# Kernel tuning notes

Measured on AMD Instinct MI355X. Metric: run time of the kernel, lower is better.

The kernel has to match this reference:

```python
import jax, jax.numpy as jnp
import numpy as np

LOCAL_EMB = 16  # local_emb_size: neighbors gathered per point


def _linear_params(key, fan_in, fan_out):
    kw, kb = jax.random.split(key)
    lim = 1.0 / np.sqrt(fan_in)
    W = jax.random.uniform(kw, (fan_in, fan_out), minval=-lim, maxval=lim, dtype=jnp.float32)
    b = jax.random.uniform(kb, (fan_out,), minval=-lim, maxval=lim, dtype=jnp.float32)
    return W, b


def setup_inputs() -> dict:
    key = jax.random.key(0)
    ks = jax.random.split(key, 4)
    M, K = 1024, 128
    windows = jax.random.normal(ks[0], (M, K, 3), dtype=jnp.float32)
    W1, b1 = _linear_params(ks[1], 3, 32)
    W2, b2 = _linear_params(ks[2], 32, 64)
    W3, b3 = _linear_params(ks[3], 64, 128)
    return {"windows": windows, "W1": W1, "b1": b1, "W2": W2, "b2": b2, "W3": W3, "b3": b3}


def reference(windows, W1, b1, W2, b2, W3, b3):
    # windows: (M, K, 3)
    M, K, _ = windows.shape
    # --- knn_points(windows, windows, K=LOCAL_EMB): per-window pairwise sq dists ---
    sq = jnp.sum(windows * windows, axis=-1)                      # (M, K)
    d2 = sq[:, :, None] + sq[:, None, :] - 2.0 * jnp.einsum('mkc,mjc->mkj', windows, windows)  # (M,K,K)
    _, idx = jax.lax.top_k(-d2, LOCAL_EMB)                        # (M, K, LOCAL_EMB) nearest (incl. self)
    grouped = jax.vmap(lambda pts, i: pts[i])(windows, idx)       # (M, K, LOCAL_EMB, 3)
    # --- center on query point ---
    rel = grouped - windows[:, :, None, :]                        # (M, K, LOCAL_EMB, 3)
    # --- n_scale_batch: normalize each neighborhood by its max radius ---
    scale = jnp.max(jnp.linalg.norm(rel, axis=-1), axis=-1, keepdims=True)  # (M, K, 1)
    rel = rel / jnp.maximum(scale, 1e-8)[..., None]
    # --- GraphConv: per-neighbor MLP stack then max over neighbors ---
    h = jax.nn.relu(rel @ W1 + b1)                                # (M, K, LOCAL_EMB, 32)
    h = jax.nn.relu(h @ W2 + b2)                                  # (M, K, LOCAL_EMB, 64)
    h = h @ W3 + b3                                               # (M, K, LOCAL_EMB, 128)
    return jnp.max(h, axis=-2)                                    # (M, K, 128)
```

## Files before the change

kernel.cpp:

```cpp
#include <hip/hip_runtime.h>

typedef __bf16 bf16x8 __attribute__((ext_vector_type(8)));
typedef __bf16 bf16x2 __attribute__((ext_vector_type(2)));
typedef float  f32x4  __attribute__((ext_vector_type(4)));
typedef float  f32x2  __attribute__((ext_vector_type(2)));
typedef unsigned long long u64;

#define MFMA(a, b, c) __builtin_amdgcn_mfma_f32_16x16x32_bf16((a), (b), (c), 0, 0, 0)

__device__ __forceinline__ f32x2 fma2(f32x2 a, f32x2 b, f32x2 c) {
    return __builtin_elementwise_fma(a, b, c);
}
__device__ __forceinline__ f32x2 relu2(f32x2 a) {
    f32x2 z = {0.0f, 0.0f};
    return __builtin_elementwise_max(a, z);
}
__device__ __forceinline__ void hilo2(f32x2 h, unsigned& hiw, unsigned& low) {
    bf16x2 hb = __builtin_convertvector(h, bf16x2);
    unsigned hw = __builtin_bit_cast(unsigned, hb);
    f32x2 hf;
    hf[0] = __builtin_bit_cast(float, hw << 16);
    hf[1] = __builtin_bit_cast(float, hw & 0xFFFF0000u);
    f32x2 lo = h - hf;
    bf16x2 lb = __builtin_convertvector(lo, bf16x2);
    hiw = hw;
    low = __builtin_bit_cast(unsigned, lb);
}
__device__ __forceinline__ bf16x8 frag4(unsigned w0, unsigned w1, unsigned w2, unsigned w3) {
    uint4 u; u.x = w0; u.y = w1; u.z = w2; u.w = w3;
    return __builtin_bit_cast(bf16x8, u);
}

__global__ __launch_bounds__(256) void miniemb_kernel(
    const float* __restrict__ windows,
    const float* __restrict__ W1, const float* __restrict__ b1,
    const float* __restrict__ W2, const float* __restrict__ b2,
    const float* __restrict__ W3, const float* __restrict__ b3,
    float* __restrict__ out)
{
    __shared__ float relbuf[48 * 128];
    __shared__ uint4 w3lds[16][64];

    float (*pts4)[4] = reinterpret_cast<float(*)[4]>(&w3lds[0][0]);

    const int m    = blockIdx.x;
    const int tid  = threadIdx.x;
    const int w    = tid >> 6;
    const int lane = tid & 63;
    const int g    = lane >> 4;
    const int ln   = lane & 15;

    const float* wm = windows + (size_t)m * 128 * 3;
    if (tid < 128) {
        float x = wm[tid * 3], y = wm[tid * 3 + 1], z = wm[tid * 3 + 2];
        float s = __fadd_rn(__fadd_rn(__fmul_rn(x, x), __fmul_rn(y, y)),
                            __fmul_rn(z, z));
        f32x4 P = {x, y, z, s};
        *(f32x4*)&pts4[tid][0] = P;
    }
    __syncthreads();

    const int k = tid >> 1;
    const int h = tid & 1;
    f32x4 Q = *(const f32x4*)&pts4[k][0];
    u64 bd[16];
    #pragma unroll
    for (int t = 0; t < 16; ++t) bd[t] = ~0ull;
    #pragma unroll 1
    for (int jj = 0; jj < 64; ++jj) {
        const int j = (h << 6) + jj;
        f32x4 P = *(const f32x4*)&pts4[j][0];
        float dot = __fadd_rn(__fadd_rn(__fmul_rn(Q.x, P.x),
                                        __fmul_rn(Q.y, P.y)),
                              __fmul_rn(Q.z, P.z));
        float dd = __fsub_rn(__fadd_rn(Q.w, P.w), __fmul_rn(2.0f, dot));
        unsigned u = __float_as_uint(dd);
        unsigned key32 = u ^ (((unsigned)(((int)u) >> 31)) | 0x80000000u);
        u64 kk = ((u64)key32 << 32) | (unsigned)j;
        bool ct[16];
        #pragma unroll
        for (int t = 0; t < 16; ++t) ct[t] = bd[t] < kk;
        #pragma unroll
        for (int t = 15; t >= 1; --t)
            bd[t] = ct[t] ? bd[t] : (ct[t - 1] ? kk : bd[t - 1]);
        bd[0] = ct[0] ? bd[0] : kk;
    }

    unsigned msk = 0;
    #pragma unroll
    for (int i = 0; i < 16; ++i) {
        u64 o = __shfl_xor(bd[15 - i], 1);
        msk |= (bd[i] < o) ? (1u << i) : 0u;
    }
    const int cnt   = __popc(msk);
    const int rbase = h ? (16 - cnt) : 0;

    float m2 = 0.0f;
    #pragma unroll
    for (int i = 0; i < 16; ++i) {
        if (i < cnt) {
            f32x4 P = *(const f32x4*)&pts4[(unsigned)bd[i] & 127u][0];
            float dx = P.x - Q.x, dy = P.y - Q.y, dz = P.z - Q.z;
            m2 = fmaxf(m2, dx * dx + dy * dy + dz * dz);
        }
    }
    m2 = fmaxf(m2, __shfl_xor(m2, 1));
    const float inv = 1.0f / fmaxf(sqrtf(m2), 1e-8f);

    #pragma unroll
    for (int i = 0; i < 16; ++i) {
        if (i < cnt) {
            f32x4 P = *(const f32x4*)&pts4[(unsigned)bd[i] & 127u][0];
            const int t0 = (rbase + i) * 3;
            relbuf[(t0 + 0) * 128 + (k ^ ((t0 + 0) & 31))] = (P.x - Q.x) * inv;
            relbuf[(t0 + 1) * 128 + (k ^ ((t0 + 1) & 31))] = (P.y - Q.y) * inv;
            relbuf[(t0 + 2) * 128 + (k ^ ((t0 + 2) & 31))] = (P.z - Q.z) * inv;
        }
    }
    __syncthreads();

    #pragma unroll
    for (int q = 0; q < 4; ++q) {
        const int f = w * 4 + q, n = f >> 1, kb = f & 1;
        bf16x8 v;
        #pragma unroll
        for (int j = 0; j < 8; ++j)
            v[j] = (__bf16)W3[(kb * 32 + g * 8 + j) * 128 + n * 16 + ln];
        w3lds[f][lane] = __builtin_bit_cast(uint4, v);
    }

    bf16x8 w2A[4];
    #pragma unroll
    for (int t = 0; t < 4; ++t) {
        const int c = 32 * (t >> 1) + 8 * (ln >> 2) + 4 * (t & 1) + (ln & 3);
        #pragma unroll
        for (int j = 0; j < 8; ++j)
            w2A[t][j] = (__bf16)W2[(g * 8 + j) * 64 + c];
    }
    float b2p[16];
    #pragma unroll
    for (int t = 0; t < 4; ++t)
        #pragma unroll
        for (int r = 0; r < 4; ++r)
            b2p[t * 4 + r] = b2[32 * (t >> 1) + 8 * g + 4 * (t & 1) + r];
    f32x2 w1v0[4], w1v1[4], w1v2[4], b1v[4];
    #pragma unroll
    for (int jj = 0; jj < 4; ++jj) {
        const int c = g * 8 + 2 * jj;
        w1v0[jj] = *(const f32x2*)&W1[c];
        w1v1[jj] = *(const f32x2*)&W1[32 + c];
        w1v2[jj] = *(const f32x2*)&W1[64 + c];
        b1v[jj]  = *(const f32x2*)&b1[c];
    }
    const float b3r0 = b3[(2 * g) * 16 + ln];
    const float b3r1 = b3[(2 * g + 1) * 16 + ln];
    __syncthreads();

    const float* ra = relbuf + (ln * 3 + 0) * 128;
    const float* rb = relbuf + (ln * 3 + 1) * 128;
    const float* rc = relbuf + (ln * 3 + 2) * 128;
    const int xa = (ln * 3 + 0) & 31;
    const int xb = (ln * 3 + 1) & 31;
    const int xc = (ln * 3 + 2) & 31;

    #pragma unroll 1
    for (int i = 0; i < 16; ++i) {
        const int p0 = w * 32 + 2 * i;
        const int p1 = p0 + 1;
        const float r00 = ra[p0 ^ xa], r01 = rb[p0 ^ xb], r02 = rc[p0 ^ xc];
        const float r10 = ra[p1 ^ xa], r11 = rb[p1 ^ xb], r12 = rc[p1 ^ xc];
        const f32x2 r00v = {r00, r00}, r01v = {r01, r01}, r02v = {r02, r02};
        const f32x2 r10v = {r10, r10}, r11v = {r11, r11}, r12v = {r12, r12};

        unsigned h0w[4], l0w[4], h1w[4], l1w[4];
        #pragma unroll
        for (int jj = 0; jj < 4; ++jj) {
            f32x2 hv0 = fma2(r02v, w1v2[jj], fma2(r01v, w1v1[jj], fma2(r00v, w1v0[jj], b1v[jj])));
            hilo2(relu2(hv0), h0w[jj], l0w[jj]);
            f32x2 hv1 = fma2(r12v, w1v2[jj], fma2(r11v, w1v1[jj], fma2(r10v, w1v0[jj], b1v[jj])));
            hilo2(relu2(hv1), h1w[jj], l1w[jj]);
        }
        bf16x8 a1hi0 = frag4(h0w[0], h0w[1], h0w[2], h0w[3]);
        bf16x8 a1lo0 = frag4(l0w[0], l0w[1], l0w[2], l0w[3]);
        bf16x8 a1hi1 = frag4(h1w[0], h1w[1], h1w[2], h1w[3]);
        bf16x8 a1lo1 = frag4(l1w[0], l1w[1], l1w[2], l1w[3]);

        f32x4 c2_0[4], c2_1[4];
        #pragma unroll
        for (int t = 0; t < 4; ++t) {
            f32x4 acc0 = {b2p[t*4+0], b2p[t*4+1], b2p[t*4+2], b2p[t*4+3]};
            f32x4 acc1 = acc0;
            acc0 = MFMA(w2A[t], a1hi0, acc0);
            acc1 = MFMA(w2A[t], a1hi1, acc1);
            acc0 = MFMA(w2A[t], a1lo0, acc0);
            acc1 = MFMA(w2A[t], a1lo1, acc1);
            c2_0[t] = acc0; c2_1[t] = acc1;
        }

        unsigned ha0[4], la0[4], hb0[4], lb0[4];
        unsigned ha1[4], la1[4], hb1[4], lb1[4];
        #pragma unroll
        for (int t = 0; t < 2; ++t) {
            f32x2 pA0 = {c2_0[t][0], c2_0[t][1]};
            f32x2 pB0 = {c2_0[t][2], c2_0[t][3]};
            hilo2(relu2(pA0), ha0[2*t],     la0[2*t]);
            hilo2(relu2(pB0), ha0[2*t + 1], la0[2*t + 1]);
            f32x2 pA0b = {c2_0[t+2][0], c2_0[t+2][1]};
            f32x2 pB0b = {c2_0[t+2][2], c2_0[t+2][3]};
            hilo2(relu2(pA0b), hb0[2*t],     lb0[2*t]);
            hilo2(relu2(pB0b), hb0[2*t + 1], lb0[2*t + 1]);
            f32x2 pA1 = {c2_1[t][0], c2_1[t][1]};
            f32x2 pB1 = {c2_1[t][2], c2_1[t][3]};
            hilo2(relu2(pA1), ha1[2*t],     la1[2*t]);
            hilo2(relu2(pB1), ha1[2*t + 1], la1[2*t + 1]);
            f32x2 pA1b = {c2_1[t+2][0], c2_1[t+2][1]};
            f32x2 pB1b = {c2_1[t+2][2], c2_1[t+2][3]};
            hilo2(relu2(pA1b), hb1[2*t],     lb1[2*t]);
            hilo2(relu2(pB1b), hb1[2*t + 1], lb1[2*t + 1]);
        }
        bf16x8 h30a = frag4(ha0[0], ha0[1], ha0[2], ha0[3]);
        bf16x8 l30a = frag4(la0[0], la0[1], la0[2], la0[3]);
        bf16x8 h30b = frag4(hb0[0], hb0[1], hb0[2], hb0[3]);
        bf16x8 l30b = frag4(lb0[0], lb0[1], lb0[2], lb0[3]);
        bf16x8 h31a = frag4(ha1[0], ha1[1], ha1[2], ha1[3]);
        bf16x8 l31a = frag4(la1[0], la1[1], la1[2], la1[3]);
        bf16x8 h31b = frag4(hb1[0], hb1[1], hb1[2], hb1[3]);
        bf16x8 l31b = frag4(lb1[0], lb1[1], lb1[2], lb1[3]);

        float s0_0 = 0.f, s1_0 = 0.f, s0_1 = 0.f, s1_1 = 0.f;
        #pragma unroll
        for (int nn = 0; nn < 4; ++nn) {
            bf16x8 c0a = __builtin_bit_cast(bf16x8, w3lds[nn * 4 + 0][lane]);
            bf16x8 c0b = __builtin_bit_cast(bf16x8, w3lds[nn * 4 + 1][lane]);
            bf16x8 c1a = __builtin_bit_cast(bf16x8, w3lds[nn * 4 + 2][lane]);
            bf16x8 c1b = __builtin_bit_cast(bf16x8, w3lds[nn * 4 + 3][lane]);
            f32x4 a00 = {0,0,0,0}, a01 = {0,0,0,0}, a10 = {0,0,0,0}, a11 = {0,0,0,0};
            a00 = MFMA(h30a, c0a, a00); a00 = MFMA(h30b, c0b, a00);
            a00 = MFMA(l30a, c0a, a00); a00 = MFMA(l30b, c0b, a00);
            a01 = MFMA(h30a, c1a, a01); a01 = MFMA(h30b, c1b, a01);
            a01 = MFMA(l30a, c1a, a01); a01 = MFMA(l30b, c1b, a01);
            a10 = MFMA(h31a, c0a, a10); a10 = MFMA(h31b, c0b, a10);
            a10 = MFMA(l31a, c0a, a10); a10 = MFMA(l31b, c0b, a10);
            a11 = MFMA(h31a, c1a, a11); a11 = MFMA(h31b, c1b, a11);
            a11 = MFMA(l31a, c1a, a11); a11 = MFMA(l31b, c1b, a11);
            f32x2 m00 = __builtin_elementwise_max((f32x2){a00[0], a00[1]}, (f32x2){a00[2], a00[3]});
            float v00 = fmaxf(m00[0], m00[1]);
            v00 = fmaxf(v00, __shfl_xor(v00, 16)); v00 = fmaxf(v00, __shfl_xor(v00, 32));
            f32x2 m01 = __builtin_elementwise_max((f32x2){a01[0], a01[1]}, (f32x2){a01[2], a01[3]});
            float v01 = fmaxf(m01[0], m01[1]);
            v01 = fmaxf(v01, __shfl_xor(v01, 16)); v01 = fmaxf(v01, __shfl_xor(v01, 32));
            f32x2 m10 = __builtin_elementwise_max((f32x2){a10[0], a10[1]}, (f32x2){a10[2], a10[3]});
            float v10 = fmaxf(m10[0], m10[1]);
            v10 = fmaxf(v10, __shfl_xor(v10, 16)); v10 = fmaxf(v10, __shfl_xor(v10, 32));
            f32x2 m11 = __builtin_elementwise_max((f32x2){a11[0], a11[1]}, (f32x2){a11[2], a11[3]});
            float v11 = fmaxf(m11[0], m11[1]);
            v11 = fmaxf(v11, __shfl_xor(v11, 16)); v11 = fmaxf(v11, __shfl_xor(v11, 32));
            if (nn == g) { s0_0 = v00; s1_0 = v01; s0_1 = v10; s1_1 = v11; }
        }
        float* o0 = out + ((size_t)(m * 128 + p0) << 7);
        float* o1 = out + ((size_t)(m * 128 + p1) << 7);
        o0[(2 * g) * 16 + ln]     = s0_0 + b3r0;
        o0[(2 * g + 1) * 16 + ln] = s1_0 + b3r1;
        o1[(2 * g) * 16 + ln]     = s0_1 + b3r0;
        o1[(2 * g + 1) * 16 + ln] = s1_1 + b3r1;
    }
}

extern "C" void kernel_launch(void* const* d_in, const int* in_sizes, int n_in,
                              void* d_out, int out_size, void* d_ws, size_t ws_size,
                              hipStream_t stream) {
    const float* windows = (const float*)d_in[0];
    const float* W1 = (const float*)d_in[1];
    const float* b1 = (const float*)d_in[2];
    const float* W2 = (const float*)d_in[3];
    const float* b2 = (const float*)d_in[4];
    const float* W3 = (const float*)d_in[5];
    const float* b3 = (const float*)d_in[6];
    float* out = (float*)d_out;
    hipLaunchKernelGGL(miniemb_kernel, dim3(1024), dim3(256), 0, stream,
                       windows, W1, b1, W2, b2, W3, b3, out);
}
```

Baseline: 214.7 us.

## Skip self-neighbor row, move W1/b1/b2 to LDS, raise occupancy to 4 blocks

The self point is always one of its own nearest neighbours, so its relative offset is zero. The kernel now drops that row from relbuf, shrinking it to 45 rows, and lane 0 feeds zeros into the first layer instead. W1, b1 and b2 move from per-thread registers into a small shared buffer that is re-read every loop iteration. This cuts register pressure so that __launch_bounds__(256,4) can allow more resident blocks per CU, at the cost of extra LDS reads in the inner loop. Correctness depends on the self point being reliably placed first by the rbase/hs ordering logic.

```diff
diff --git a/kernel.cpp b/kernel.cpp
--- a/kernel.cpp
+++ b/kernel.cpp
@@ -31,14 +31,15 @@
     return __builtin_bit_cast(bf16x8, u);
 }
 
-__global__ __launch_bounds__(256) void miniemb_kernel(
+__global__ __launch_bounds__(256, 4) void miniemb_kernel(
     const float* __restrict__ windows,
     const float* __restrict__ W1, const float* __restrict__ b1,
     const float* __restrict__ W2, const float* __restrict__ b2,
     const float* __restrict__ W3, const float* __restrict__ b3,
     float* __restrict__ out)
 {
-    __shared__ float relbuf[48 * 128];
+    __shared__ float relbuf[45 * 128];
+    __shared__ float wlds[192];
     __shared__ uint4 w3lds[16][64];
 
     float (*pts4)[4] = reinterpret_cast<float(*)[4]>(&w3lds[0][0]);
@@ -58,6 +59,8 @@
         f32x4 P = {x, y, z, s};
         *(f32x4*)&pts4[tid][0] = P;
     }
+    if (tid < 192)
+        wlds[tid] = (tid < 96) ? W1[tid] : (tid < 128 ? b1[tid - 96] : b2[tid - 128]);
     __syncthreads();
 
     const int k = tid >> 1;
@@ -93,7 +96,8 @@
         msk |= (bd[i] < o) ? (1u << i) : 0u;
     }
     const int cnt   = __popc(msk);
-    const int rbase = h ? (16 - cnt) : 0;
+    const int hs    = k >> 6;
+    const int rbase = (h == hs) ? 0 : (16 - cnt);
 
     float m2 = 0.0f;
     #pragma unroll
@@ -110,11 +114,14 @@
     #pragma unroll
     for (int i = 0; i < 16; ++i) {
         if (i < cnt) {
-            f32x4 P = *(const f32x4*)&pts4[(unsigned)bd[i] & 127u][0];
-            const int t0 = (rbase + i) * 3;
-            relbuf[(t0 + 0) * 128 + (k ^ ((t0 + 0) & 31))] = (P.x - Q.x) * inv;
-            relbuf[(t0 + 1) * 128 + (k ^ ((t0 + 1) & 31))] = (P.y - Q.y) * inv;
-            relbuf[(t0 + 2) * 128 + (k ^ ((t0 + 2) & 31))] = (P.z - Q.z) * inv;
+            const int row = rbase + i;
+            if (row > 0) {
+                f32x4 P = *(const f32x4*)&pts4[(unsigned)bd[i] & 127u][0];
+                const int t0 = (row - 1) * 3;
+                relbuf[(t0 + 0) * 128 + (k ^ ((t0 + 0) & 31))] = (P.x - Q.x) * inv;
+                relbuf[(t0 + 1) * 128 + (k ^ ((t0 + 1) & 31))] = (P.y - Q.y) * inv;
+                relbuf[(t0 + 2) * 128 + (k ^ ((t0 + 2) & 31))] = (P.z - Q.z) * inv;
+            }
         }
     }
     __syncthreads();
@@ -137,47 +144,46 @@
         for (int j = 0; j < 8; ++j)
             w2A[t][j] = (__bf16)W2[(g * 8 + j) * 64 + c];
     }
-    float b2p[16];
-    #pragma unroll
-    for (int t = 0; t < 4; ++t)
-        #pragma unroll
-        for (int r = 0; r < 4; ++r)
-            b2p[t * 4 + r] = b2[32 * (t >> 1) + 8 * g + 4 * (t & 1) + r];
-    f32x2 w1v0[4], w1v1[4], w1v2[4], b1v[4];
-    #pragma unroll
-    for (int jj = 0; jj < 4; ++jj) {
-        const int c = g * 8 + 2 * jj;
-        w1v0[jj] = *(const f32x2*)&W1[c];
-        w1v1[jj] = *(const f32x2*)&W1[32 + c];
-        w1v2[jj] = *(const f32x2*)&W1[64 + c];
-        b1v[jj]  = *(const f32x2*)&b1[c];
-    }
     const float b3r0 = b3[(2 * g) * 16 + ln];
     const float b3r1 = b3[(2 * g + 1) * 16 + ln];
     __syncthreads();
 
-    const float* ra = relbuf + (ln * 3 + 0) * 128;
-    const float* rb = relbuf + (ln * 3 + 1) * 128;
-    const float* rc = relbuf + (ln * 3 + 2) * 128;
-    const int xa = (ln * 3 + 0) & 31;
-    const int xb = (ln * 3 + 1) & 31;
-    const int xc = (ln * 3 + 2) & 31;
+    const int lnm = (ln == 0) ? 0 : (ln - 1);
+    const float* ra = relbuf + (lnm * 3 + 0) * 128;
+    const float* rb = relbuf + (lnm * 3 + 1) * 128;
+    const float* rc = relbuf + (lnm * 3 + 2) * 128;
+    const int xa = (lnm * 3 + 0) & 31;
+    const int xb = (lnm * 3 + 1) & 31;
+    const int xc = (lnm * 3 + 2) & 31;
+    const float* w1p = wlds + g * 8;
+    const float* b2g = wlds + 128 + 8 * g;
 
     #pragma unroll 1
     for (int i = 0; i < 16; ++i) {
         const int p0 = w * 32 + 2 * i;
         const int p1 = p0 + 1;
-        const float r00 = ra[p0 ^ xa], r01 = rb[p0 ^ xb], r02 = rc[p0 ^ xc];
-        const float r10 = ra[p1 ^ xa], r11 = rb[p1 ^ xb], r12 = rc[p1 ^ xc];
+        float r00 = ra[p0 ^ xa], r01 = rb[p0 ^ xb], r02 = rc[p0 ^ xc];
+        float r10 = ra[p1 ^ xa], r11 = rb[p1 ^ xb], r12 = rc[p1 ^ xc];
+        if (ln == 0) { r00 = 0.f; r01 = 0.f; r02 = 0.f; r10 = 0.f; r11 = 0.f; r12 = 0.f; }
         const f32x2 r00v = {r00, r00}, r01v = {r01, r01}, r02v = {r02, r02};
         const f32x2 r10v = {r10, r10}, r11v = {r11, r11}, r12v = {r12, r12};
 
+        f32x4 W0A = *(const f32x4*)&w1p[0],   W0B = *(const f32x4*)&w1p[4];
+        f32x4 W1A = *(const f32x4*)&w1p[32],  W1B = *(const f32x4*)&w1p[36];
+        f32x4 W2A_ = *(const f32x4*)&w1p[64], W2B_ = *(const f32x4*)&w1p[68];
+        f32x4 BA  = *(const f32x4*)&w1p[96],  BB  = *(const f32x4*)&w1p[100];
+
         unsigned h0w[4], l0w[4], h1w[4], l1w[4];
         #pragma unroll
         for (int jj = 0; jj < 4; ++jj) {
-            f32x2 hv0 = fma2(r02v, w1v2[jj], fma2(r01v, w1v1[jj], fma2(r00v, w1v0[jj], b1v[jj])));
+            const int e = 2 * (jj & 1);
+            f32x2 w0 = (jj < 2) ? (f32x2){W0A[e], W0A[e+1]} : (f32x2){W0B[e], W0B[e+1]};
+            f32x2 w1 = (jj < 2) ? (f32x2){W1A[e], W1A[e+1]} : (f32x2){W1B[e], W1B[e+1]};
+            f32x2 w2 = (jj < 2) ? (f32x2){W2A_[e], W2A_[e+1]} : (f32x2){W2B_[e], W2B_[e+1]};
+            f32x2 bb = (jj < 2) ? (f32x2){BA[e], BA[e+1]} : (f32x2){BB[e], BB[e+1]};
+            f32x2 hv0 = fma2(r02v, w2, fma2(r01v, w1, fma2(r00v, w0, bb)));
             hilo2(relu2(hv0), h0w[jj], l0w[jj]);
-            f32x2 hv1 = fma2(r12v, w1v2[jj], fma2(r11v, w1v1[jj], fma2(r10v, w1v0[jj], b1v[jj])));
+            f32x2 hv1 = fma2(r12v, w2, fma2(r11v, w1, fma2(r10v, w0, bb)));
             hilo2(relu2(hv1), h1w[jj], l1w[jj]);
         }
         bf16x8 a1hi0 = frag4(h0w[0], h0w[1], h0w[2], h0w[3]);
@@ -188,7 +194,7 @@
         f32x4 c2_0[4], c2_1[4];
         #pragma unroll
         for (int t = 0; t < 4; ++t) {
-            f32x4 acc0 = {b2p[t*4+0], b2p[t*4+1], b2p[t*4+2], b2p[t*4+3]};
+            f32x4 acc0 = *(const f32x4*)&b2g[32 * (t >> 1) + 4 * (t & 1)];
             f32x4 acc1 = acc0;
             acc0 = MFMA(w2A[t], a1hi0, acc0);
             acc1 = MFMA(w2A[t], a1hi1, acc1);
```

Result: slower. 270.2 us (+25.8%).
